# Optimization experiments

Measured on AMD Instinct MI355X. Metric: run time of the kernel, lower is better.

Reference implementation:

```python
import jax, jax.numpy as jnp
import numpy as np

N_NODES = 1024
H = 256        # hidden_dim
HEADS = 4
EPS = 1e-5     # torch LayerNorm default


def _ln(x, g, b):
    m = x.mean(-1, keepdims=True)
    v = ((x - m) ** 2).mean(-1, keepdims=True)
    return (x - m) / jnp.sqrt(v + EPS) * g + b


def setup_inputs() -> dict:
    key = jax.random.key(0)
    ks = jax.random.split(key, 24)
    B, L = 16, 64
    P = N_NODES * (N_NODES - 1) // 2
    D0 = L + 7  # latent_dim + 7 stats
    s = 0.02
    f32 = jnp.float32
    d = {}
    d['x'] = jax.random.normal(ks[0], (B, L), f32)
    d['stats'] = jax.random.normal(ks[1], (B, 7), f32)
    d['u'] = jax.random.uniform(ks[2], (B, P, 2), f32)  # uniform noise -> gumbel
    d['ln0_g'] = jnp.ones((D0,), f32); d['ln0_b'] = jnp.zeros((D0,), f32)
    # residual block 1 (in D0 -> H, has projection)
    d['rb1_ln_g'] = jnp.ones((D0,), f32); d['rb1_ln_b'] = jnp.zeros((D0,), f32)
    d['rb1_w1'] = jax.random.normal(ks[3], (H, D0), f32) * s; d['rb1_b1'] = jnp.zeros((H,), f32)
    d['rb1_w2'] = jax.random.normal(ks[4], (H, H), f32) * s;  d['rb1_b2'] = jnp.zeros((H,), f32)
    d['rb1_wp'] = jax.random.normal(ks[5], (H, D0), f32) * s; d['rb1_bp'] = jnp.zeros((H,), f32)
    # residual block 2 (H -> H, no projection)
    d['rb2_ln_g'] = jnp.ones((H,), f32); d['rb2_ln_b'] = jnp.zeros((H,), f32)
    d['rb2_w1'] = jax.random.normal(ks[6], (H, H), f32) * s; d['rb2_b1'] = jnp.zeros((H,), f32)
    d['rb2_w2'] = jax.random.normal(ks[7], (H, H), f32) * s; d['rb2_b2'] = jnp.zeros((H,), f32)
    # GraphAttention: LN + MHA(in_proj, out_proj) + output Linear
    d['att_ln_g'] = jnp.ones((H,), f32); d['att_ln_b'] = jnp.zeros((H,), f32)
    d['att_win'] = jax.random.normal(ks[8], (3 * H, H), f32) * s; d['att_bin'] = jnp.zeros((3 * H,), f32)
    d['att_wout'] = jax.random.normal(ks[9], (H, H), f32) * s;    d['att_bout'] = jnp.zeros((H,), f32)
    d['out_w'] = jax.random.normal(ks[10], (H, H), f32) * s;      d['out_b'] = jnp.zeros((H,), f32)
    # final edge-logit layer over concat([h_i, h_j]) -> 2
    d['fin_w'] = jax.random.normal(ks[11], (2, 2 * H), f32) * s;  d['fin_b'] = jnp.zeros((2,), f32)
    d['temp'] = jnp.ones((1,), f32)
    return d


def reference(x, stats, u, ln0_g, ln0_b,
              rb1_ln_g, rb1_ln_b, rb1_w1, rb1_b1, rb1_w2, rb1_b2, rb1_wp, rb1_bp,
              rb2_ln_g, rb2_ln_b, rb2_w1, rb2_b1, rb2_w2, rb2_b2,
              att_ln_g, att_ln_b, att_win, att_bin, att_wout, att_bout,
              out_w, out_b, fin_w, fin_b, temp):
    B = x.shape[0]
    z = jnp.concatenate([x, stats], axis=-1)          # [B, D0]
    z = _ln(z, ln0_g, ln0_b)
    h = jnp.broadcast_to(z[:, None, :], (B, N_NODES, z.shape[-1]))  # [B, N, D0]
    # residual block 1 (dropout in eval mode = identity)
    t = _ln(h, rb1_ln_g, rb1_ln_b)
    t = jax.nn.gelu(t @ rb1_w1.T + rb1_b1, approximate=False)
    t = t @ rb1_w2.T + rb1_b2
    h = t + (h @ rb1_wp.T + rb1_bp)                   # [B, N, H]
    # residual block 2
    t = _ln(h, rb2_ln_g, rb2_ln_b)
    t = jax.nn.gelu(t @ rb2_w1.T + rb2_b1, approximate=False)
    t = t @ rb2_w2.T + rb2_b2
    h = t + h
    # GraphAttention: LN -> self MHA -> output linear
    a = _ln(h, att_ln_g, att_ln_b)
    qkv = a @ att_win.T + att_bin                      # [B, N, 3H]
    q, k, v = jnp.split(qkv, 3, axis=-1)
    dh = H // HEADS
    def heads(t):
        return t.reshape(B, N_NODES, HEADS, dh).transpose(0, 2, 1, 3)
    q, k, v = heads(q), heads(k), heads(v)
    scores = jnp.einsum('bhqd,bhkd->bhqk', q, k) * np.float32(1.0 / np.sqrt(dh))
    att = jax.nn.softmax(scores, axis=-1)
    o = jnp.einsum('bhqk,bhkd->bhqd', att, v).transpose(0, 2, 1, 3).reshape(B, N_NODES, H)
    o = o @ att_wout.T + att_bout
    h = o @ out_w.T + out_b                            # [B, N, H]
    # pairwise edge logits: Linear(cat(h_i, h_j)) == h_i @ W_a^T + h_j @ W_b^T + b
    la = h @ fin_w[:, :H].T                            # [B, N, 2]
    lb = h @ fin_w[:, H:].T                            # [B, N, 2]
    iu, ju = jnp.triu_indices(N_NODES, k=1)
    logits = la[:, iu] + lb[:, ju] + fin_b             # [B, P, 2]
    # gumbel-softmax (hard, straight-through), tau = |temperature|
    tau = jnp.abs(temp)[0]
    g = -jnp.log(-jnp.log(u + 1e-10) + 1e-10)
    y_soft = jax.nn.softmax((logits + g) / tau, axis=-1)
    y_hard = jax.nn.one_hot(jnp.argmax(y_soft, axis=-1), 2, dtype=y_soft.dtype)
    y = y_hard + y_soft - jax.lax.stop_gradient(y_soft)
    e = y[..., 0]                                      # [B, P]
    adj = jnp.zeros((B, N_NODES, N_NODES), e.dtype).at[:, iu, ju].set(e)
    return adj + adj.transpose(0, 2, 1)
```

## Files before the change

kernel.cpp:

```cpp
#include <hip/hip_runtime.h>
#include <math.h>


#define NN    1024
#define HD    256
#define DIN0  71
#define NPAIR 523776
#define TILE  64
#define NT    16
#define HT    1024

__device__ __forceinline__ double blk_reduce(double v, double* red) {
  #pragma unroll
  for (int m = 32; m > 0; m >>= 1) v += __shfl_xor(v, m, 64);
  const int wid = threadIdx.x >> 6;
  __syncthreads();
  if ((threadIdx.x & 63) == 0) red[wid] = v;
  __syncthreads();
  double s = 0.0;
  #pragma unroll
  for (int w = 0; w < HT / 64; ++w) s += red[w];
  return s;
}

__device__ __forceinline__ void ln_to(const double* src, double* dst, int D,
                                      const float* __restrict__ gam,
                                      const float* __restrict__ bet,
                                      double* red) {
  const int tid = threadIdx.x;
  double v = (tid < D) ? src[tid] : 0.0;
  double m = blk_reduce(v, red) / (double)D;
  double d = (tid < D) ? (src[tid] - m) : 0.0;
  double var = blk_reduce(d * d, red) / (double)D;
  double inv = 1.0 / sqrt(var + (double)1e-5f);
  if (tid < D) dst[tid] = d * inv * (double)gam[tid] + (double)bet[tid];
  __syncthreads();
}

__device__ __forceinline__ double dot4_256(const double* src,
                                           const float* __restrict__ W,
                                           int row, int p) {
  const float4* w4 = reinterpret_cast<const float4*>(W + (size_t)row * 256);
  double a0 = 0.0, a1 = 0.0, a2 = 0.0, a3 = 0.0;
  #pragma unroll
  for (int k = 0; k < 16; ++k) {
    const int f = p + 4 * k;
    float4 w = w4[f];
    const double* s = src + 4 * f;
    a0 += s[0] * (double)w.x;
    a1 += s[1] * (double)w.y;
    a2 += s[2] * (double)w.z;
    a3 += s[3] * (double)w.w;
  }
  return (a0 + a1) + (a2 + a3);
}

__device__ __forceinline__ double dot4_71(const double* src,
                                          const float* __restrict__ W,
                                          int row, int p) {
  const float* wr = W + (size_t)row * DIN0;
  double a = 0.0;
  #pragma unroll
  for (int i = p; i < DIN0; i += 4) a += src[i] * (double)wr[i];
  return a;
}

__device__ __forceinline__ double quad_sum(double v) {
  v += __shfl_xor(v, 1, 64);
  v += __shfl_xor(v, 2, 64);
  return v;
}

__device__ __forceinline__ double gelu_exact(double x) {
  return 0.5 * x * (1.0 + erf(x * 0.70710678118654752440));
}

__global__ __launch_bounds__(HT)
void head_kernel(const float* __restrict__ x, const float* __restrict__ stats,
                 const float* __restrict__ ln0_g, const float* __restrict__ ln0_b,
                 const float* __restrict__ rb1_ln_g, const float* __restrict__ rb1_ln_b,
                 const float* __restrict__ rb1_w1, const float* __restrict__ rb1_b1,
                 const float* __restrict__ rb1_w2, const float* __restrict__ rb1_b2,
                 const float* __restrict__ rb1_wp, const float* __restrict__ rb1_bp,
                 const float* __restrict__ rb2_ln_g, const float* __restrict__ rb2_ln_b,
                 const float* __restrict__ rb2_w1, const float* __restrict__ rb2_b1,
                 const float* __restrict__ rb2_w2, const float* __restrict__ rb2_b2,
                 const float* __restrict__ att_ln_g, const float* __restrict__ att_ln_b,
                 const float* __restrict__ att_win, const float* __restrict__ att_bin,
                 const float* __restrict__ att_wout, const float* __restrict__ att_bout,
                 const float* __restrict__ out_w, const float* __restrict__ out_b,
                 const float* __restrict__ fin_w, const float* __restrict__ fin_b,
                 double* __restrict__ c_out) {
  __shared__ double h[HD], t[HD], g[HD], red[HT / 64];
  const int tid = threadIdx.x;
  const int b = blockIdx.x;
  const int r = tid >> 2;
  const int p = tid & 3;

  if (tid < DIN0)
    h[tid] = (tid < 64) ? (double)x[b * 64 + tid] : (double)stats[b * 7 + tid - 64];
  __syncthreads();

  ln_to(h, h, DIN0, ln0_g, ln0_b, red);

  ln_to(h, t, DIN0, rb1_ln_g, rb1_ln_b, red);
  {
    double d = quad_sum(dot4_71(t, rb1_w1, r, p));
    if (p == 0) g[r] = gelu_exact(d + (double)rb1_b1[r]);
  }
  __syncthreads();
  {
    double d2 = quad_sum(dot4_256(g, rb1_w2, r, p));
    double dp = quad_sum(dot4_71(h, rb1_wp, r, p));
    __syncthreads();
    if (p == 0) h[r] = (d2 + (double)rb1_b2[r]) + (dp + (double)rb1_bp[r]);
  }
  __syncthreads();

  ln_to(h, t, HD, rb2_ln_g, rb2_ln_b, red);
  {
    double d = quad_sum(dot4_256(t, rb2_w1, r, p));
    if (p == 0) g[r] = gelu_exact(d + (double)rb2_b1[r]);
  }
  __syncthreads();
  {
    double d = quad_sum(dot4_256(g, rb2_w2, r, p));
    if (p == 0) h[r] = h[r] + (d + (double)rb2_b2[r]);
  }
  __syncthreads();

  ln_to(h, t, HD, att_ln_g, att_ln_b, red);
  {
    double d = quad_sum(dot4_256(t, att_win + 2 * HD * HD, r, p));
    if (p == 0) g[r] = d + (double)att_bin[2 * HD + r];
  }
  __syncthreads();
  {
    double d = quad_sum(dot4_256(g, att_wout, r, p));
    if (p == 0) t[r] = d + (double)att_bout[r];
  }
  __syncthreads();
  {
    double d = quad_sum(dot4_256(t, out_w, r, p));
    if (p == 0) g[r] = d + (double)out_b[r];
  }
  __syncthreads();

  double v0 = 0.0, v1 = 0.0;
  if (tid < HD) {
    const double hj = g[tid];
    v0 = hj * (double)fin_w[tid]          + hj * (double)fin_w[HD + tid];
    v1 = hj * (double)fin_w[2 * HD + tid] + hj * (double)fin_w[3 * HD + tid];
  }
  double c0 = blk_reduce(v0, red) + (double)fin_b[0];
  double c1 = blk_reduce(v1, red) + (double)fin_b[1];
  if (tid == 0) {
    c_out[2 * b + 0] = c0;
    c_out[2 * b + 1] = c1;
  }
}

__global__ __launch_bounds__(256)
void adj_tile_kernel(const float* __restrict__ u, const double* __restrict__ c,
                     float* __restrict__ out) {
  __shared__ float tile[TILE][TILE + 1];
  const int b = blockIdx.y;
  int k = blockIdx.x;
  int ti = 0;
  while (k >= NT - ti) { k -= NT - ti; ++ti; }
  const int tj = ti + k;
  const bool diag = (ti == tj);

  const int t        = threadIdx.x;
  const int lane_col = (t & 15) << 2;
  const int row_base = t >> 4;
  const double c0 = c[2 * b + 0];
  const double c1 = c[2 * b + 1];
  const float* ub = u + (size_t)b * (2u * NPAIR);
  float* ob = out + ((size_t)b << 20);

  #pragma unroll
  for (int s = 0; s < 4; ++s) {
    const int il = s * 16 + row_base;
    const int i  = ti * TILE + il;
    const int rb = i * (2 * NN - 1 - i) / 2 - i - 1;
    float4 ev4;
    float* ev = &ev4.x;
    #pragma unroll
    for (int q = 0; q < 4; ++q) {
      const int jl = lane_col + q;
      const int j  = tj * TILE + jl;
      float e = 0.0f;
      if (j > i) {
        const int p2 = rb + j;
        const float2 uu = *reinterpret_cast<const float2*>(ub + 2 * p2);
        const float g0 = -logf(-logf(uu.x + 1e-10f) + 1e-10f);
        const float g1 = -logf(-logf(uu.y + 1e-10f) + 1e-10f);
        e = ((c0 + (double)g0) >= (c1 + (double)g1)) ? 1.0f : 0.0f;
      }
      ev[q] = e;
      tile[il][jl] = e;
    }
    if (!diag) {
      *reinterpret_cast<float4*>(ob + (size_t)i * NN + tj * TILE + lane_col) = ev4;
    }
  }
  __syncthreads();

  #pragma unroll
  for (int s = 0; s < 4; ++s) {
    const int rl = s * 16 + row_base;
    if (!diag) {
      float4 v = make_float4(tile[lane_col + 0][rl], tile[lane_col + 1][rl],
                             tile[lane_col + 2][rl], tile[lane_col + 3][rl]);
      *reinterpret_cast<float4*>(ob + (size_t)(tj * TILE + rl) * NN
                                    + ti * TILE + lane_col) = v;
    } else {
      float v[4];
      #pragma unroll
      for (int q = 0; q < 4; ++q) {
        const int jl = lane_col + q;
        v[q] = (jl > rl) ? tile[rl][jl] : ((jl < rl) ? tile[jl][rl] : 0.0f);
      }
      *reinterpret_cast<float4*>(ob + (size_t)(ti * TILE + rl) * NN
                                    + ti * TILE + lane_col)
          = make_float4(v[0], v[1], v[2], v[3]);
    }
  }
}

extern "C" void kernel_launch(void* const* d_in, const int* in_sizes, int n_in,
                              void* d_out, int out_size, void* d_ws, size_t ws_size,
                              hipStream_t stream) {
  const float* x        = (const float*)d_in[0];
  const float* stats    = (const float*)d_in[1];
  const float* u        = (const float*)d_in[2];
  const float* ln0_g    = (const float*)d_in[3];
  const float* ln0_b    = (const float*)d_in[4];
  const float* rb1_ln_g = (const float*)d_in[5];
  const float* rb1_ln_b = (const float*)d_in[6];
  const float* rb1_w1   = (const float*)d_in[7];
  const float* rb1_b1   = (const float*)d_in[8];
  const float* rb1_w2   = (const float*)d_in[9];
  const float* rb1_b2   = (const float*)d_in[10];
  const float* rb1_wp   = (const float*)d_in[11];
  const float* rb1_bp   = (const float*)d_in[12];
  const float* rb2_ln_g = (const float*)d_in[13];
  const float* rb2_ln_b = (const float*)d_in[14];
  const float* rb2_w1   = (const float*)d_in[15];
  const float* rb2_b1   = (const float*)d_in[16];
  const float* rb2_w2   = (const float*)d_in[17];
  const float* rb2_b2   = (const float*)d_in[18];
  const float* att_ln_g = (const float*)d_in[19];
  const float* att_ln_b = (const float*)d_in[20];
  const float* att_win  = (const float*)d_in[21];
  const float* att_bin  = (const float*)d_in[22];
  const float* att_wout = (const float*)d_in[23];
  const float* att_bout = (const float*)d_in[24];
  const float* out_w    = (const float*)d_in[25];
  const float* out_b    = (const float*)d_in[26];
  const float* fin_w    = (const float*)d_in[27];
  const float* fin_b    = (const float*)d_in[28];

  double* c_ws = (double*)d_ws;
  float* out   = (float*)d_out;

  hipLaunchKernelGGL(head_kernel, dim3(16), dim3(HT), 0, stream,
                     x, stats, ln0_g, ln0_b,
                     rb1_ln_g, rb1_ln_b, rb1_w1, rb1_b1, rb1_w2, rb1_b2, rb1_wp, rb1_bp,
                     rb2_ln_g, rb2_ln_b, rb2_w1, rb2_b1, rb2_w2, rb2_b2,
                     att_ln_g, att_ln_b, att_win, att_bin, att_wout, att_bout,
                     out_w, out_b, fin_w, fin_b, c_ws);

  hipLaunchKernelGGL(adj_tile_kernel, dim3(NT * (NT + 1) / 2, 16), dim3(256), 0, stream,
                     u, c_ws, out);
}
```

Measured before the change: 236.4 us.

## Split serial head MLP kernel into per-layer kernels over row groups

The single head kernel, with 16 blocks of 1024 threads, ran the whole MLP/attention chain one block per batch. It is replaced by a chain of per-layer kernels, each launching 64 blocks of 256 threads that split the output rows into four groups. Intermediate activations go through scratch space at the tail of the output buffer. This spreads the serial head computation over more compute units, at the cost of extra kernel launches, recomputing LN0 in two kernels, and round trips through global memory between layers.

```diff
diff --git a/kernel.cpp b/kernel.cpp
--- a/kernel.cpp
+++ b/kernel.cpp
@@ -8,61 +8,15 @@
 #define NPAIR 523776
 #define TILE  64
 #define NT    16
-#define HT    1024
-
-__device__ __forceinline__ double blk_reduce(double v, double* red) {
+
+__device__ __forceinline__ double bred(double v, double* red4) {
   #pragma unroll
   for (int m = 32; m > 0; m >>= 1) v += __shfl_xor(v, m, 64);
   const int wid = threadIdx.x >> 6;
   __syncthreads();
-  if ((threadIdx.x & 63) == 0) red[wid] = v;
-  __syncthreads();
-  double s = 0.0;
-  #pragma unroll
-  for (int w = 0; w < HT / 64; ++w) s += red[w];
-  return s;
-}
-
-__device__ __forceinline__ void ln_to(const double* src, double* dst, int D,
-                                      const float* __restrict__ gam,
-                                      const float* __restrict__ bet,
-                                      double* red) {
-  const int tid = threadIdx.x;
-  double v = (tid < D) ? src[tid] : 0.0;
-  double m = blk_reduce(v, red) / (double)D;
-  double d = (tid < D) ? (src[tid] - m) : 0.0;
-  double var = blk_reduce(d * d, red) / (double)D;
-  double inv = 1.0 / sqrt(var + (double)1e-5f);
-  if (tid < D) dst[tid] = d * inv * (double)gam[tid] + (double)bet[tid];
-  __syncthreads();
-}
-
-__device__ __forceinline__ double dot4_256(const double* src,
-                                           const float* __restrict__ W,
-                                           int row, int p) {
-  const float4* w4 = reinterpret_cast<const float4*>(W + (size_t)row * 256);
-  double a0 = 0.0, a1 = 0.0, a2 = 0.0, a3 = 0.0;
-  #pragma unroll
-  for (int k = 0; k < 16; ++k) {
-    const int f = p + 4 * k;
-    float4 w = w4[f];
-    const double* s = src + 4 * f;
-    a0 += s[0] * (double)w.x;
-    a1 += s[1] * (double)w.y;
-    a2 += s[2] * (double)w.z;
-    a3 += s[3] * (double)w.w;
-  }
-  return (a0 + a1) + (a2 + a3);
-}
-
-__device__ __forceinline__ double dot4_71(const double* src,
-                                          const float* __restrict__ W,
-                                          int row, int p) {
-  const float* wr = W + (size_t)row * DIN0;
-  double a = 0.0;
-  #pragma unroll
-  for (int i = p; i < DIN0; i += 4) a += src[i] * (double)wr[i];
-  return a;
+  if ((threadIdx.x & 63) == 0) red4[wid] = v;
+  __syncthreads();
+  return (red4[0] + red4[1]) + (red4[2] + red4[3]);
 }
 
 __device__ __forceinline__ double quad_sum(double v) {
@@ -71,89 +25,158 @@
   return v;
 }
 
+__device__ __forceinline__ double dotq256(const double* s,
+                                          const float* __restrict__ W,
+                                          int row, int p) {
+  const float4* w4 = reinterpret_cast<const float4*>(W + (size_t)row * 256);
+  double a0 = 0.0, a1 = 0.0, a2 = 0.0, a3 = 0.0;
+  #pragma unroll
+  for (int k = 0; k < 16; ++k) {
+    const int f = p + 4 * k;
+    float4 w = w4[f];
+    const double* sp = s + 4 * f;
+    a0 += sp[0] * (double)w.x;
+    a1 += sp[1] * (double)w.y;
+    a2 += sp[2] * (double)w.z;
+    a3 += sp[3] * (double)w.w;
+  }
+  return (a0 + a1) + (a2 + a3);
+}
+
+__device__ __forceinline__ double dotq71(const double* s,
+                                         const float* __restrict__ W,
+                                         int row, int p) {
+  const float* wr = W + (size_t)row * DIN0;
+  double a = 0.0;
+  #pragma unroll
+  for (int i = p; i < DIN0; i += 4) a += s[i] * (double)wr[i];
+  return a;
+}
+
 __device__ __forceinline__ double gelu_exact(double x) {
   return 0.5 * x * (1.0 + erf(x * 0.70710678118654752440));
 }
 
-__global__ __launch_bounds__(HT)
-void head_kernel(const float* __restrict__ x, const float* __restrict__ stats,
-                 const float* __restrict__ ln0_g, const float* __restrict__ ln0_b,
-                 const float* __restrict__ rb1_ln_g, const float* __restrict__ rb1_ln_b,
-                 const float* __restrict__ rb1_w1, const float* __restrict__ rb1_b1,
-                 const float* __restrict__ rb1_w2, const float* __restrict__ rb1_b2,
-                 const float* __restrict__ rb1_wp, const float* __restrict__ rb1_bp,
-                 const float* __restrict__ rb2_ln_g, const float* __restrict__ rb2_ln_b,
-                 const float* __restrict__ rb2_w1, const float* __restrict__ rb2_b1,
-                 const float* __restrict__ rb2_w2, const float* __restrict__ rb2_b2,
-                 const float* __restrict__ att_ln_g, const float* __restrict__ att_ln_b,
-                 const float* __restrict__ att_win, const float* __restrict__ att_bin,
-                 const float* __restrict__ att_wout, const float* __restrict__ att_bout,
-                 const float* __restrict__ out_w, const float* __restrict__ out_b,
-                 const float* __restrict__ fin_w, const float* __restrict__ fin_b,
-                 double* __restrict__ c_out) {
-  __shared__ double h[HD], t[HD], g[HD], red[HT / 64];
-  const int tid = threadIdx.x;
+__device__ __forceinline__ void ln0_into(const float* __restrict__ x,
+                                         const float* __restrict__ stats,
+                                         const float* __restrict__ g,
+                                         const float* __restrict__ bb,
+                                         int b, double* h0, double* red4) {
+  const int tid = threadIdx.x;
+  double z = 0.0;
+  if (tid < DIN0)
+    z = (tid < 64) ? (double)x[b * 64 + tid] : (double)stats[b * 7 + tid - 64];
+  const double m = bred((tid < DIN0) ? z : 0.0, red4) / (double)DIN0;
+  const double d = (tid < DIN0) ? (z - m) : 0.0;
+  const double var = bred(d * d, red4) / (double)DIN0;
+  const double inv = 1.0 / sqrt(var + (double)1e-5f);
+  if (tid < DIN0) h0[tid] = d * inv * (double)g[tid] + (double)bb[tid];
+  __syncthreads();
+}
+
+__global__ __launch_bounds__(256)
+void k1_ln_w1(const float* __restrict__ x, const float* __restrict__ stats,
+              const float* __restrict__ ln0_g, const float* __restrict__ ln0_b,
+              const float* __restrict__ l1g, const float* __restrict__ l1b,
+              const float* __restrict__ W1, const float* __restrict__ b1,
+              double* __restrict__ G) {
+  __shared__ double t[DIN0], red[4];
+  const int b = blockIdx.x >> 2, rg = blockIdx.x & 3;
+  const int tid = threadIdx.x;
+  ln0_into(x, stats, ln0_g, ln0_b, b, t, red);
+  {
+    double v = (tid < DIN0) ? t[tid] : 0.0;
+    const double m = bred(v, red) / (double)DIN0;
+    const double d = (tid < DIN0) ? (t[tid] - m) : 0.0;
+    const double var = bred(d * d, red) / (double)DIN0;
+    const double inv = 1.0 / sqrt(var + (double)1e-5f);
+    __syncthreads();
+    if (tid < DIN0) t[tid] = d * inv * (double)l1g[tid] + (double)l1b[tid];
+    __syncthreads();
+  }
+  const int row = rg * 64 + (tid >> 2), p = tid & 3;
+  const double d = quad_sum(dotq71(t, W1, row, p));
+  if (p == 0) G[b * HD + row] = gelu_exact(d + (double)b1[row]);
+}
+
+__global__ __launch_bounds__(256)
+void k2_w2_wp(const float* __restrict__ x, const float* __restrict__ stats,
+              const float* __restrict__ ln0_g, const float* __restrict__ ln0_b,
+              const float* __restrict__ W2, const float* __restrict__ b2,
+              const float* __restrict__ Wp, const float* __restrict__ bp,
+              const double* __restrict__ G, double* __restrict__ H) {
+  __shared__ double h0[DIN0], gs[HD], red[4];
+  const int b = blockIdx.x >> 2, rg = blockIdx.x & 3;
+  const int tid = threadIdx.x;
+  gs[tid] = G[b * HD + tid];
+  ln0_into(x, stats, ln0_g, ln0_b, b, h0, red);
+  const int row = rg * 64 + (tid >> 2), p = tid & 3;
+  const double d2 = quad_sum(dotq256(gs, W2, row, p));
+  const double dp = quad_sum(dotq71(h0, Wp, row, p));
+  if (p == 0)
+    H[b * HD + row] = (d2 + (double)b2[row]) + (dp + (double)bp[row]);
+}
+
+__global__ __launch_bounds__(256)
+void k3_ln_mv(const double* __restrict__ S,
+              const float* __restrict__ lg, const float* __restrict__ lb,
+              const float* __restrict__ W, const float* __restrict__ bb,
+              double* __restrict__ D, int gelu_flag) {
+  __shared__ double t[HD], red[4];
+  const int b = blockIdx.x >> 2, rg = blockIdx.x & 3;
+  const int tid = threadIdx.x;
+  const double s = S[b * HD + tid];
+  const double m = bred(s, red) / (double)HD;
+  const double d = s - m;
+  const double var = bred(d * d, red) / (double)HD;
+  const double inv = 1.0 / sqrt(var + (double)1e-5f);
+  t[tid] = d * inv * (double)lg[tid] + (double)lb[tid];
+  __syncthreads();
+  const int row = rg * 64 + (tid >> 2), p = tid & 3;
+  const double dd = quad_sum(dotq256(t, W, row, p));
+  if (p == 0) {
+    const double v = dd + (double)bb[row];
+    D[b * HD + row] = gelu_flag ? gelu_exact(v) : v;
+  }
+}
+
+__global__ __launch_bounds__(256)
+void k4_mv_res(const double* __restrict__ G, const float* __restrict__ W,
+               const float* __restrict__ bb, double* __restrict__ H) {
+  __shared__ double gs[HD];
+  const int b = blockIdx.x >> 2, rg = blockIdx.x & 3;
+  const int tid = threadIdx.x;
+  gs[tid] = G[b * HD + tid];
+  __syncthreads();
+  const int row = rg * 64 + (tid >> 2), p = tid & 3;
+  const double d = quad_sum(dotq256(gs, W, row, p));
+  if (p == 0) H[b * HD + row] += d + (double)bb[row];
+}
+
+__global__ __launch_bounds__(256)
+void k5_mv(const double* __restrict__ S, const float* __restrict__ W,
+           const float* __restrict__ bb, double* __restrict__ D) {
+  __shared__ double ss[HD];
+  const int b = blockIdx.x >> 2, rg = blockIdx.x & 3;
+  const int tid = threadIdx.x;
+  ss[tid] = S[b * HD + tid];
+  __syncthreads();
+  const int row = rg * 64 + (tid >> 2), p = tid & 3;
+  const double d = quad_sum(dotq256(ss, W, row, p));
+  if (p == 0) D[b * HD + row] = d + (double)bb[row];
+}
+
+__global__ __launch_bounds__(256)
+void k6_fin(const double* __restrict__ Hf, const float* __restrict__ fin_w,
+            const float* __restrict__ fin_b, double* __restrict__ c_out) {
+  __shared__ double red[4];
   const int b = blockIdx.x;
-  const int r = tid >> 2;
-  const int p = tid & 3;
-
-  if (tid < DIN0)
-    h[tid] = (tid < 64) ? (double)x[b * 64 + tid] : (double)stats[b * 7 + tid - 64];
-  __syncthreads();
-
-  ln_to(h, h, DIN0, ln0_g, ln0_b, red);
-
-  ln_to(h, t, DIN0, rb1_ln_g, rb1_ln_b, red);
-  {
-    double d = quad_sum(dot4_71(t, rb1_w1, r, p));
-    if (p == 0) g[r] = gelu_exact(d + (double)rb1_b1[r]);
-  }
-  __syncthreads();
-  {
-    double d2 = quad_sum(dot4_256(g, rb1_w2, r, p));
-    double dp = quad_sum(dot4_71(h, rb1_wp, r, p));
-    __syncthreads();
-    if (p == 0) h[r] = (d2 + (double)rb1_b2[r]) + (dp + (double)rb1_bp[r]);
-  }
-  __syncthreads();
-
-  ln_to(h, t, HD, rb2_ln_g, rb2_ln_b, red);
-  {
-    double d = quad_sum(dot4_256(t, rb2_w1, r, p));
-    if (p == 0) g[r] = gelu_exact(d + (double)rb2_b1[r]);
-  }
-  __syncthreads();
-  {
-    double d = quad_sum(dot4_256(g, rb2_w2, r, p));
-    if (p == 0) h[r] = h[r] + (d + (double)rb2_b2[r]);
-  }
-  __syncthreads();
-
-  ln_to(h, t, HD, att_ln_g, att_ln_b, red);
-  {
-    double d = quad_sum(dot4_256(t, att_win + 2 * HD * HD, r, p));
-    if (p == 0) g[r] = d + (double)att_bin[2 * HD + r];
-  }
-  __syncthreads();
-  {
-    double d = quad_sum(dot4_256(g, att_wout, r, p));
-    if (p == 0) t[r] = d + (double)att_bout[r];
-  }
-  __syncthreads();
-  {
-    double d = quad_sum(dot4_256(t, out_w, r, p));
-    if (p == 0) g[r] = d + (double)out_b[r];
-  }
-  __syncthreads();
-
-  double v0 = 0.0, v1 = 0.0;
-  if (tid < HD) {
-    const double hj = g[tid];
-    v0 = hj * (double)fin_w[tid]          + hj * (double)fin_w[HD + tid];
-    v1 = hj * (double)fin_w[2 * HD + tid] + hj * (double)fin_w[3 * HD + tid];
-  }
-  double c0 = blk_reduce(v0, red) + (double)fin_b[0];
-  double c1 = blk_reduce(v1, red) + (double)fin_b[1];
+  const int tid = threadIdx.x;
+  const double hj = Hf[b * HD + tid];
+  const double v0 = hj * (double)fin_w[tid]          + hj * (double)fin_w[HD + tid];
+  const double v1 = hj * (double)fin_w[2 * HD + tid] + hj * (double)fin_w[3 * HD + tid];
+  const double c0 = bred(v0, red) + (double)fin_b[0];
+  const double c1 = bred(v1, red) + (double)fin_b[1];
   if (tid == 0) {
     c_out[2 * b + 0] = c0;
     c_out[2 * b + 1] = c1;
@@ -262,16 +285,31 @@
   const float* fin_w    = (const float*)d_in[27];
   const float* fin_b    = (const float*)d_in[28];
 
+  float* out   = (float*)d_out;
   double* c_ws = (double*)d_ws;
-  float* out   = (float*)d_out;
-
-  hipLaunchKernelGGL(head_kernel, dim3(16), dim3(HT), 0, stream,
-                     x, stats, ln0_g, ln0_b,
-                     rb1_ln_g, rb1_ln_b, rb1_w1, rb1_b1, rb1_w2, rb1_b2, rb1_wp, rb1_bp,
-                     rb2_ln_g, rb2_ln_b, rb2_w1, rb2_b1, rb2_w2, rb2_b2,
-                     att_ln_g, att_ln_b, att_win, att_bin, att_wout, att_bout,
-                     out_w, out_b, fin_w, fin_b, c_ws);
-
-  hipLaunchKernelGGL(adj_tile_kernel, dim3(NT * (NT + 1) / 2, 16), dim3(256), 0, stream,
+
+  double* G = (double*)(out + ((size_t)16 * NN * NN - 3 * 16 * HD * 2));
+  double* H = G + 16 * HD;
+  double* T = H + 16 * HD;
+
+  const dim3 g64(64), t256(256);
+  hipLaunchKernelGGL(k1_ln_w1, g64, t256, 0, stream,
+                     x, stats, ln0_g, ln0_b, rb1_ln_g, rb1_ln_b,
+                     rb1_w1, rb1_b1, G);
+  hipLaunchKernelGGL(k2_w2_wp, g64, t256, 0, stream,
+                     x, stats, ln0_g, ln0_b, rb1_w2, rb1_b2, rb1_wp, rb1_bp,
+                     G, H);
+  hipLaunchKernelGGL(k3_ln_mv, g64, t256, 0, stream,
+                     H, rb2_ln_g, rb2_ln_b, rb2_w1, rb2_b1, G, 1);
+  hipLaunchKernelGGL(k4_mv_res, g64, t256, 0, stream,
+                     G, rb2_w2, rb2_b2, H);
+  hipLaunchKernelGGL(k3_ln_mv, g64, t256, 0, stream,
+                     H, att_ln_g, att_ln_b, att_win + 2 * HD * HD,
+                     att_bin + 2 * HD, G, 0);
+  hipLaunchKernelGGL(k5_mv, g64, t256, 0, stream, G, att_wout, att_bout, T);
+  hipLaunchKernelGGL(k5_mv, g64, t256, 0, stream, T, out_w, out_b, G);
+  hipLaunchKernelGGL(k6_fin, dim3(16), t256, 0, stream, G, fin_w, fin_b, c_ws);
+
+  hipLaunchKernelGGL(adj_tile_kernel, dim3(NT * (NT + 1) / 2, 16), t256, 0, stream,
                      u, c_ws, out);
 }
```

New measurement: 223.6 us. 1.06x faster.
